# Kernel optimization log

Measured on AMD Instinct MI355X. Metric: run time of the kernel, lower is better.

## Reference

```python
import jax, jax.numpy as jnp
import numpy as np

H_WIN, W_WIN = 5, 5
PADH, PADW = H_WIN // 2, W_WIN // 2
SIGMA = 1.0
GAUSS_DEN = 2.0 * SIGMA ** 2
NCLASSES = 20


def setup_inputs() -> dict:
    key = jax.random.key(0)
    k1, k2, k3 = jax.random.split(key, 3)
    xyz = jax.random.normal(k1, (2, 3, 64, 2048), dtype=jnp.float32)
    softmax = jax.random.uniform(k2, (2, 20, 64, 2048), dtype=jnp.float32)
    mask = jax.random.randint(k3, (2, 64, 2048), 0, 2, dtype=jnp.int32)
    return {"xyz": xyz, "softmax": softmax, "mask": mask}


def _window_indices(H, W):
    # rows: zero-padded in height (like F.unfold padding), cols: circular in width
    dh = jnp.arange(-PADH, PADH + 1)
    rows = jnp.arange(H)[:, None] + dh              # (H, h)
    valid = (rows >= 0) & (rows < H)                # (H, h)
    rows_c = jnp.clip(rows, 0, H - 1)
    dw = jnp.arange(-PADW, PADW + 1)
    cols = (jnp.arange(W)[:, None] + dw) % W        # (W, w) circular
    return rows_c, valid, cols


def _gather_windows(a, rows_c, valid, cols):
    # a: (..., H, W) -> (..., H, h, W, w); out-of-range rows -> 0 (zero padding)
    g = a[..., rows_c, :]                           # (..., H, h, W)
    g = jnp.where(valid[:, :, None], g, jnp.zeros((), a.dtype))
    return g[..., cols]                             # (..., H, h, W, w)


def reference(xyz, softmax, mask):
    N, C, H, W = softmax.shape
    sm = softmax * mask.astype(softmax.dtype)[:, None]   # mask invalid pixels
    rows_c, valid, cols = _window_indices(H, W)

    x, y, z = xyz[:, 0], xyz[:, 1], xyz[:, 2]            # each (N, H, W)
    wx = _gather_windows(x, rows_c, valid, cols)         # (N, H, h, W, w)
    wy = _gather_windows(y, rows_c, valid, cols)
    wz = _gather_windows(z, rows_c, valid, cols)
    cx = x[:, :, None, :, None]
    cy = y[:, :, None, :, None]
    cz = z[:, :, None, :, None]
    dist2 = (wx - cx) ** 2 + (wy - cy) ** 2 + (wz - cz) ** 2
    gauss = jnp.exp(-dist2 / GAUSS_DEN)                  # (N, H, h, W, w)

    sm_w = _gather_windows(sm, rows_c, valid, cols)      # (N, C, H, h, W, w)
    out = (sm_w * gauss[:, None]).sum(axis=(3, 5))       # (N, C, H, W)
    return out
```

## Files before the change

### kernel.cpp

```cpp
#include <hip/hip_runtime.h>

constexpr int N = 2;
constexpr int C = 20;
constexpr int H = 64;
constexpr int W = 2048;
constexpr int HW = H * W;

constexpr int BLK  = 256;
constexpr int OPT  = 2;
constexpr int TILE = BLK * OPT;

__global__ __launch_bounds__(BLK, 2)
void lcl_xyz_kernel(const float* __restrict__ xyz,
                    const float* __restrict__ softmax,
                    const int* __restrict__ mask,
                    float* __restrict__ out) {
    const int t = threadIdx.x;

    const int bid  = blockIdx.x;
    const int work = (bid & 7) * 64 + (bid >> 3);
    const int nh   = work >> 2;
    const int bw   = work & 3;
    const int n    = nh >> 6;
    const int h    = nh & 63;
    const int w    = bw * TILE + 2 * t;

    int  rowoff[5];
    bool hv[5];
    #pragma unroll
    for (int r = 0; r < 5; ++r) {
        int hh = h - 2 + r;
        hv[r] = (unsigned)hh < (unsigned)H;
        rowoff[r] = min(max(hh, 0), H - 1) * W;
    }

    const int cm = (w - 2) & (W - 1);
    const int c0 = w;
    const int cp = (w + 2) & (W - 1);

    const float* xb = xyz + (size_t)(n * 3 + 0) * HW;
    const float* yb = xyz + (size_t)(n * 3 + 1) * HW;
    const float* zb = xyz + (size_t)(n * 3 + 2) * HW;
    const int*   mb = mask + (size_t)n * HW;

    const float2 cx2 = *(const float2*)(xb + h * W + c0);
    const float2 cy2 = *(const float2*)(yb + h * W + c0);
    const float2 cz2 = *(const float2*)(zb + h * W + c0);

    float wa[5][5], wb_[5][5];
    #pragma unroll
    for (int r = 0; r < 5; ++r) {
        float2 xm = *(const float2*)(xb + rowoff[r] + cm);
        float2 x0 = *(const float2*)(xb + rowoff[r] + c0);
        float2 xp = *(const float2*)(xb + rowoff[r] + cp);
        float2 ym = *(const float2*)(yb + rowoff[r] + cm);
        float2 y0 = *(const float2*)(yb + rowoff[r] + c0);
        float2 yp = *(const float2*)(yb + rowoff[r] + cp);
        float2 zm = *(const float2*)(zb + rowoff[r] + cm);
        float2 z0 = *(const float2*)(zb + rowoff[r] + c0);
        float2 zp = *(const float2*)(zb + rowoff[r] + cp);
        int2   km = *(const int2*)(mb + rowoff[r] + cm);
        int2   k0 = *(const int2*)(mb + rowoff[r] + c0);
        int2   kp = *(const int2*)(mb + rowoff[r] + cp);

        const float xv[6] = {xm.x, xm.y, x0.x, x0.y, xp.x, xp.y};
        const float yv[6] = {ym.x, ym.y, y0.x, y0.y, yp.x, yp.y};
        const float zv[6] = {zm.x, zm.y, z0.x, z0.y, zp.x, zp.y};
        const int   mv[6] = {km.x, km.y, k0.x, k0.y, kp.x, kp.y};

        #pragma unroll
        for (int j = 0; j < 5; ++j) {
            {
                float dx = xv[j] - cx2.x, dy = yv[j] - cy2.x, dz = zv[j] - cz2.x;
                float g  = __expf(-0.5f * (dx * dx + dy * dy + dz * dz));
                wa[r][j] = (hv[r] && mv[j]) ? g : 0.0f;
            }
            {
                float dx = xv[j + 1] - cx2.y, dy = yv[j + 1] - cy2.y, dz = zv[j + 1] - cz2.y;
                float g  = __expf(-0.5f * (dx * dx + dy * dy + dz * dz));
                wb_[r][j] = (hv[r] && mv[j + 1]) ? g : 0.0f;
            }
        }
    }

    const float* smb = softmax + (size_t)n * C * HW;
    float*       ob  = out + (size_t)n * C * HW + (size_t)h * W + w;

    float2 A0[5], A1[5], A2[5];
    float2 B0[5], B1[5], B2[5];

#define LOADS(b0, b1, b2, c)                                              \
    do {                                                                  \
        const float* sc = smb + (size_t)(c) * HW;                         \
        _Pragma("unroll")                                                 \
        for (int r = 0; r < 5; ++r) {                                     \
            b0[r] = *(const float2*)(sc + rowoff[r] + cm);                \
            b1[r] = *(const float2*)(sc + rowoff[r] + c0);                \
            b2[r] = *(const float2*)(sc + rowoff[r] + cp);                \
        }                                                                 \
    } while (0)

#define COMP(b0, b1, b2, c)                                               \
    do {                                                                  \
        float a0 = 0.0f, a1 = 0.0f;                                       \
        _Pragma("unroll")                                                 \
        for (int r = 0; r < 5; ++r) {                                     \
            float v0 = b0[r].x, v1 = b0[r].y;                             \
            float v2 = b1[r].x, v3 = b1[r].y;                             \
            float v4 = b2[r].x, v5 = b2[r].y;                             \
            a0 = fmaf(wa[r][0], v0, a0);                                  \
            a0 = fmaf(wa[r][1], v1, a0);                                  \
            a0 = fmaf(wa[r][2], v2, a0);                                  \
            a0 = fmaf(wa[r][3], v3, a0);                                  \
            a0 = fmaf(wa[r][4], v4, a0);                                  \
            a1 = fmaf(wb_[r][0], v1, a1);                                 \
            a1 = fmaf(wb_[r][1], v2, a1);                                 \
            a1 = fmaf(wb_[r][2], v3, a1);                                 \
            a1 = fmaf(wb_[r][3], v4, a1);                                 \
            a1 = fmaf(wb_[r][4], v5, a1);                                 \
        }                                                                 \
        float2 o; o.x = a0; o.y = a1;                                     \
        *(float2*)(ob + (size_t)(c) * HW) = o;                            \
    } while (0)

    LOADS(A0, A1, A2, 0);
    #pragma unroll
    for (int c = 0; c < C; c += 2) {
        LOADS(B0, B1, B2, c + 1);
        COMP(A0, A1, A2, c);
        if (c + 2 < C) LOADS(A0, A1, A2, c + 2);
        COMP(B0, B1, B2, c + 1);
    }
#undef LOADS
#undef COMP
}

extern "C" void kernel_launch(void* const* d_in, const int* in_sizes, int n_in,
                              void* d_out, int out_size, void* d_ws, size_t ws_size,
                              hipStream_t stream) {
    const float* xyz     = (const float*)d_in[0];
    const float* softmax = (const float*)d_in[1];
    const int*   mask    = (const int*)d_in[2];
    float*       out     = (float*)d_out;

    const int grid = N * H * (W / TILE);
    lcl_xyz_kernel<<<grid, BLK, 0, stream>>>(xyz, softmax, mask, out);
}
```

Measured before the change: 29.78 us.

## Split channels across two thread halves and double grid size

Each block now covers 256 width sites with two 128-thread halves, each handling 10 of the 20 channels, which doubles the grid to 1024 blocks. The launch-bounds occupancy hint rises from 2 to 4 blocks per CU. The intent is more parallelism and latency hiding on a GPU with many CUs, since the previous grid had only 512 blocks. In exchange the Gaussian weights, and their xyz/mask loads and exps, are computed twice per site, and the explicit double-buffered prefetch is replaced by unroll 2.

```diff
diff --git a/kernel.cpp b/kernel.cpp
--- a/kernel.cpp
+++ b/kernel.cpp
@@ -6,24 +6,25 @@
 constexpr int W = 2048;
 constexpr int HW = H * W;
 
-constexpr int BLK  = 256;
-constexpr int OPT  = 2;
-constexpr int TILE = BLK * OPT;
+constexpr int BLK   = 256;
+constexpr int SITES = 256;
 
-__global__ __launch_bounds__(BLK, 2)
+__global__ __launch_bounds__(BLK, 4)
 void lcl_xyz_kernel(const float* __restrict__ xyz,
                     const float* __restrict__ softmax,
                     const int* __restrict__ mask,
                     float* __restrict__ out) {
-    const int t = threadIdx.x;
+    const int t  = threadIdx.x;
+    const int sp = t & 127;
+    const int ch = t >> 7;
 
     const int bid  = blockIdx.x;
-    const int work = (bid & 7) * 64 + (bid >> 3);
-    const int nh   = work >> 2;
-    const int bw   = work & 3;
+    const int work = (bid & 7) * 128 + (bid >> 3);
+    const int nh   = work >> 3;
+    const int bw   = work & 7;
     const int n    = nh >> 6;
     const int h    = nh & 63;
-    const int w    = bw * TILE + 2 * t;
+    const int w    = bw * SITES + 2 * sp;
 
     int  rowoff[5];
     bool hv[5];
@@ -85,54 +86,38 @@
 
     const float* smb = softmax + (size_t)n * C * HW;
     float*       ob  = out + (size_t)n * C * HW + (size_t)h * W + w;
+    const int    cb  = ch * 10;
 
-    float2 A0[5], A1[5], A2[5];
-    float2 B0[5], B1[5], B2[5];
-
-#define LOADS(b0, b1, b2, c)                                              \
-    do {                                                                  \
-        const float* sc = smb + (size_t)(c) * HW;                         \
-        _Pragma("unroll")                                                 \
-        for (int r = 0; r < 5; ++r) {                                     \
-            b0[r] = *(const float2*)(sc + rowoff[r] + cm);                \
-            b1[r] = *(const float2*)(sc + rowoff[r] + c0);                \
-            b2[r] = *(const float2*)(sc + rowoff[r] + cp);                \
-        }                                                                 \
-    } while (0)
-
-#define COMP(b0, b1, b2, c)                                               \
-    do {                                                                  \
-        float a0 = 0.0f, a1 = 0.0f;                                       \
-        _Pragma("unroll")                                                 \
-        for (int r = 0; r < 5; ++r) {                                     \
-            float v0 = b0[r].x, v1 = b0[r].y;                             \
-            float v2 = b1[r].x, v3 = b1[r].y;                             \
-            float v4 = b2[r].x, v5 = b2[r].y;                             \
-            a0 = fmaf(wa[r][0], v0, a0);                                  \
-            a0 = fmaf(wa[r][1], v1, a0);                                  \
-            a0 = fmaf(wa[r][2], v2, a0);                                  \
-            a0 = fmaf(wa[r][3], v3, a0);                                  \
-            a0 = fmaf(wa[r][4], v4, a0);                                  \
-            a1 = fmaf(wb_[r][0], v1, a1);                                 \
-            a1 = fmaf(wb_[r][1], v2, a1);                                 \
-            a1 = fmaf(wb_[r][2], v3, a1);                                 \
-            a1 = fmaf(wb_[r][3], v4, a1);                                 \
-            a1 = fmaf(wb_[r][4], v5, a1);                                 \
-        }                                                                 \
-        float2 o; o.x = a0; o.y = a1;                                     \
-        *(float2*)(ob + (size_t)(c) * HW) = o;                            \
-    } while (0)
-
-    LOADS(A0, A1, A2, 0);
-    #pragma unroll
-    for (int c = 0; c < C; c += 2) {
-        LOADS(B0, B1, B2, c + 1);
-        COMP(A0, A1, A2, c);
-        if (c + 2 < C) LOADS(A0, A1, A2, c + 2);
-        COMP(B0, B1, B2, c + 1);
+    #pragma unroll 2
+    for (int c = cb; c < cb + 10; ++c) {
+        const float* sc = smb + (size_t)c * HW;
+        float2 b0[5], b1[5], b2[5];
+        #pragma unroll
+        for (int r = 0; r < 5; ++r) {
+            b0[r] = *(const float2*)(sc + rowoff[r] + cm);
+            b1[r] = *(const float2*)(sc + rowoff[r] + c0);
+            b2[r] = *(const float2*)(sc + rowoff[r] + cp);
+        }
+        float a0 = 0.0f, a1 = 0.0f;
+        #pragma unroll
+        for (int r = 0; r < 5; ++r) {
+            float v0 = b0[r].x, v1 = b0[r].y;
+            float v2 = b1[r].x, v3 = b1[r].y;
+            float v4 = b2[r].x, v5 = b2[r].y;
+            a0 = fmaf(wa[r][0], v0, a0);
+            a0 = fmaf(wa[r][1], v1, a0);
+            a0 = fmaf(wa[r][2], v2, a0);
+            a0 = fmaf(wa[r][3], v3, a0);
+            a0 = fmaf(wa[r][4], v4, a0);
+            a1 = fmaf(wb_[r][0], v1, a1);
+            a1 = fmaf(wb_[r][1], v2, a1);
+            a1 = fmaf(wb_[r][2], v3, a1);
+            a1 = fmaf(wb_[r][3], v4, a1);
+            a1 = fmaf(wb_[r][4], v5, a1);
+        }
+        float2 o; o.x = a0; o.y = a1;
+        *(float2*)(ob + (size_t)c * HW) = o;
     }
-#undef LOADS
-#undef COMP
 }
 
 extern "C" void kernel_launch(void* const* d_in, const int* in_sizes, int n_in,
@@ -143,6 +128,6 @@
     const int*   mask    = (const int*)d_in[2];
     float*       out     = (float*)d_out;
 
-    const int grid = N * H * (W / TILE);
+    const int grid = N * H * (W / SITES);
     lcl_xyz_kernel<<<grid, BLK, 0, stream>>>(xyz, softmax, mask, out);
 }
```

Result: slower. 79.95 us (+168.5%).
